# Kernel optimization log

Hardware: AMD Instinct MI355X
Metric: run time of the kernel (lower is better)

Reference implementation:

```python
import jax, jax.numpy as jnp
import numpy as np

B, T, I, H, N_LAYERS = 32, 1024, 512, 512, 4


def _custom_lstm(x, w, u, b):
    # x: [B,T,I]; w: [4,I,H] (gate order i,f,c,o); u: [4,H,H]; b: [4,H]
    # Preactivations for all timesteps/gates at once: [T,4,B,H]
    pre = jnp.einsum('bti,gih->tgbh', x, w) + b[None, :, None, :]
    h0 = jnp.zeros((x.shape[0], b.shape[-1]), x.dtype)
    c0 = jnp.zeros_like(h0)

    def step(carry, p):
        h, c = carry
        rec = jnp.einsum('bh,ghk->gbk', h, u)
        g = jax.nn.sigmoid(p + rec)          # all 4 gates use sigmoid (incl. g_t, as in source)
        i_t, f_t, g_t, o_t = g[0], g[1], g[2], g[3]
        c = f_t + c + i_t * g_t              # faithful: additive, not f*c
        h = o_t + jnp.tanh(c)                # faithful: additive, not o*tanh(c)
        return (h, c), h

    (h, c), hs = jax.lax.scan(step, (h0, c0), pre)
    return h, c, jnp.transpose(hs, (1, 0, 2))  # [B,T,H]


def _vlstm(x, h_prev, wx, wh, u, b):
    # x: [B,T,I]; h_prev: [B,T,H]; wx: [4,I,H]; wh: [4,H,H]; u: [4,H,H]; b: [4,H]
    # Source bug preserved: ALL gates use u[0] (u_i) and b[0] (b_i).
    pre = (jnp.einsum('bti,gih->tgbh', x, wx)
           + jnp.einsum('bth,ghk->tgbk', h_prev, wh)
           + b[0][None, None, None, :])
    u_i = u[0]
    h0 = jnp.zeros((x.shape[0], b.shape[-1]), x.dtype)
    c0 = jnp.zeros_like(h0)

    def step(carry, p):
        h, c = carry
        rec = h @ u_i                        # shared recurrent term for all gates
        g = jax.nn.sigmoid(p + rec[None])
        i_t, f_t, g_t, o_t = g[0], g[1], g[2], g[3]
        c = f_t + c + i_t * g_t
        h = o_t + jnp.tanh(c)
        return (h, c), h

    (h, c), hs = jax.lax.scan(step, (h0, c0), pre)
    return h, c, jnp.transpose(hs, (1, 0, 2))


def setup_inputs() -> dict:
    key = jax.random.key(0)
    ks = jax.random.split(key, 6)
    stdv = 1.0 / np.sqrt(H)
    u_ = lambda k, shp: jax.random.uniform(k, shp, jnp.float32, -stdv, stdv)
    L = N_LAYERS - 1
    return {
        'x': jax.random.normal(ks[0], (B, T, I), jnp.float32),
        'w1': u_(ks[1], (4, I, H)),
        'u1': u_(ks[2], (4, H, H)),
        'b1': u_(ks[3], (4, H)),
        'wx': u_(ks[4], (L, 4, I, H)),
        'wh': u_(ks[5], (L, 4, H, H)),
        'uv': u_(jax.random.fold_in(key, 10), (L, 4, H, H)),
        'bv': u_(jax.random.fold_in(key, 11), (L, 4, H)),
    }


def reference(x, w1, u1, b1, wx, wh, uv, bv):
    h_t, c_t, h_vec = _custom_lstm(x, w1, u1, b1)
    for l in range(wx.shape[0]):  # verbose path: each VLSTM sees raw x + prev layer h_vec
        h_t, c_t, h_vec = _vlstm(x, h_vec, wx[l], wh[l], uv[l], bv[l])
    return h_t, c_t, h_vec
```

## Files before the change

### kernel.cpp

```cpp
#include <hip/hip_runtime.h>

typedef unsigned short u16;
typedef unsigned int u32;
typedef unsigned long long u64;
typedef __attribute__((ext_vector_type(4))) float f32x4;
typedef __attribute__((ext_vector_type(8))) short short8;
typedef __attribute__((ext_vector_type(4))) short short4v;

__device__ __forceinline__ float bf2f(u16 v){ u32 b = ((u32)v)<<16; float f; __builtin_memcpy(&f,&b,4); return f; }
__device__ __forceinline__ u16 f2bf(float f){ u32 b; __builtin_memcpy(&b,&f,4); b = b + 0x7fffu + ((b>>16)&1u); return (u16)(b>>16); }
__device__ __forceinline__ float sigm(float x){ return 1.f/(1.f+__expf(-x)); }
__device__ __forceinline__ float tanh_a(float x){ return 1.f - 2.f/(__expf(2.f*x)+1.f); }
__device__ __forceinline__ int imin(int a, int b){ return a<b?a:b; }

typedef const __attribute__((address_space(1))) u32* gas1;
typedef __attribute__((address_space(3))) u32* las3;
__device__ __forceinline__ void gld16(const u16* g, u16* l){
  __builtin_amdgcn_global_load_lds((gas1)g, (las3)l, 16, 0, 0);
}

__device__ __forceinline__ void pub64(u32* p, u64 v){
  __hip_atomic_store((u64*)p, v, __ATOMIC_RELAXED, __HIP_MEMORY_SCOPE_AGENT);
}
__device__ __forceinline__ void pub32(u32* p, u32 v){
  __hip_atomic_store(p, v, __ATOMIC_RELAXED, __HIP_MEMORY_SCOPE_AGENT);
}
__device__ __forceinline__ u64 pol64(const u32* p){
  return __hip_atomic_load((const u64*)p, __ATOMIC_RELAXED, __HIP_MEMORY_SCOPE_AGENT);
}
__device__ __forceinline__ u32 pol32(const u32* p){
  return __hip_atomic_load(p, __ATOMIC_RELAXED, __HIP_MEMORY_SCOPE_AGENT);
}

__global__ void cast_x_kernel(const float* __restrict__ in, u16* __restrict__ out){
  int i = blockIdx.x*256 + threadIdx.x;
  for (; i < 4194304; i += 2048*256){
    f32x4 v = ((const f32x4*)in)[i];
    short4v o;
    o[0]=(short)f2bf(v[0]); o[1]=(short)f2bf(v[1]); o[2]=(short)f2bf(v[2]); o[3]=(short)f2bf(v[3]);
    ((short4v*)out)[i] = o;
  }
}

__global__ void pack_w_kernel(const float* __restrict__ w1, const float* __restrict__ wx, const float* __restrict__ wh,
                              u16* __restrict__ w1p, u16* __restrict__ wxwhp){
  int e = blockIdx.x*256 + threadIdx.x;
  for (; e < 7340032; e += 2048*256){
    if (e < 1048576){
      int h = e & 511, k = (e>>9)&511, g = e>>18;
      w1p[(size_t)(g*512+h)*512 + k] = f2bf(w1[(size_t)g*262144 + (size_t)k*512 + h]);
    } else {
      int r = e - 1048576;
      int lv = r >> 21;
      int q = r & 2097151;
      int n = q >> 10, k = q & 1023;
      int g = n >> 9, h = n & 511;
      float v;
      if (k < 512) v = wx[(size_t)lv*1048576 + (size_t)g*262144 + (size_t)k*512 + h];
      else         v = wh[(size_t)lv*1048576 + (size_t)g*262144 + (size_t)(k-512)*512 + h];
      wxwhp[(size_t)lv*2097152 + (size_t)n*1024 + k] = f2bf(v);
    }
  }
}

__global__ void cast_u_kernel(const float* __restrict__ u1, const float* __restrict__ uv,
                              u16* __restrict__ u1p, u16* __restrict__ uv0p){
  int e = blockIdx.x*256 + threadIdx.x;
  for (; e < 1835008; e += 1024*256){
    if (e < 1048576) u1p[e] = f2bf(u1[e]);
    else { int r = e - 1048576; uv0p[r] = f2bf(uv[(size_t)(r>>18)*1048576 + (r & 262143)]); }
  }
}

__global__ __launch_bounds__(256) void gemm_pre_kernel(
    const u16* __restrict__ A1, const u16* __restrict__ B1,
    const u16* __restrict__ A2, const u16* __restrict__ B2,
    const float* __restrict__ bias, int bmask,
    u16* __restrict__ Out, int nPass)
{
  __shared__ u16 As[128*64];
  __shared__ u16 Bs[128*64];
  const int tid = threadIdx.x;
  const int w = tid>>6, lane = tid&63;
  const int l15 = lane&15, l4 = lane>>4;
  const int m0 = blockIdx.x*128, n0 = blockIdx.y*128;
  const int wm = w>>1, wn = w&1;
  f32x4 acc[4][4];
#pragma unroll
  for (int a=0;a<4;a++)
#pragma unroll
    for (int bq=0;bq<4;bq++) acc[a][bq] = (f32x4){0.f,0.f,0.f,0.f};

  for (int p=0;p<nPass;p++){
    const u16* Ap = p ? A2 : A1;
    const u16* Bp = p ? B2 : B1;
    for (int kt=0;kt<8;kt++){
      const int k0 = kt*64;
      __syncthreads();
#pragma unroll
      for (int i=0;i<4;i++){
        int chunk = w*4 + i;
        int fb = chunk*1024 + lane*16;
        int row = fb>>7;
        int slot = (fb>>4)&7;
        const u16* srcA = Ap + (size_t)(m0+row)*512 + k0 + ((slot ^ (row&7))<<3);
        gld16(srcA, (u16*)As + chunk*512);
        const u16* srcB = Bp + (size_t)(n0+row)*512 + k0 + ((slot ^ (row&7))<<3);
        gld16(srcB, (u16*)Bs + chunk*512);
      }
      __syncthreads();
#pragma unroll
      for (int kk=0;kk<2;kk++){
        short8 af[4], bfq[4];
#pragma unroll
        for (int mi=0;mi<4;mi++){
          int row = wm*64 + mi*16 + l15;
          int s16 = l4 + kk*4;
          af[mi] = *(const short8*)&As[row*64 + ((s16 ^ (row&7))<<3)];
        }
#pragma unroll
        for (int ni=0;ni<4;ni++){
          int row = wn*64 + ni*16 + l15;
          int s16 = l4 + kk*4;
          bfq[ni] = *(const short8*)&Bs[row*64 + ((s16 ^ (row&7))<<3)];
        }
#pragma unroll
        for (int mi=0;mi<4;mi++)
#pragma unroll
          for (int ni=0;ni<4;ni++)
            acc[mi][ni] = __builtin_amdgcn_mfma_f32_16x16x32_bf16(af[mi], bfq[ni], acc[mi][ni], 0,0,0);
      }
    }
  }
#pragma unroll
  for (int ni=0;ni<4;ni++){
    int col = n0 + wn*64 + ni*16 + l15;
    float bb = bias[col & bmask];
#pragma unroll
    for (int mi=0;mi<4;mi++){
#pragma unroll
      for (int i=0;i<4;i++){
        int row = m0 + wm*64 + mi*16 + l4*4 + i;
        Out[(size_t)row*2048 + col] = f2bf(acc[mi][ni][i] + bb);
      }
    }
  }
}

__global__ __launch_bounds__(512,2) void mega_kernel(
    const u16* __restrict__ pre1, const u16* __restrict__ u1p,
    const u16* __restrict__ uv0p, const u16* __restrict__ xb,
    const u16* __restrict__ wxwhp, const float* __restrict__ bv,
    u32* hring, u32* pring, u32* prog, float* __restrict__ out)
{
  __shared__ char smem[33024];
  const int bid = blockIdx.x;
  const int tid = threadIdx.x;
  const int lane = tid&63, w = tid>>6;
  const int l15 = lane&15, l4 = lane>>4;

  if (bid < 16){
    u16* hs = (u16*)smem;
    float* recb = (float*)(smem+16384);
    const int gk = bid & 7, gb = bid >> 3;
    const int b0 = gb*16, kb = gk*64;
    const int g = w>>1, ch = w&1;
    short8 bfr[2][16];
#pragma unroll
    for (int n=0;n<2;n++){
      const u16* up = u1p + (size_t)g*262144 + (kb + ch*32 + n*16 + l15);
#pragma unroll
      for (int s=0;s<16;s++){
        int kbase = s*32 + l4*8;
#pragma unroll
        for (int j=0;j<8;j++) bfr[n][s][j] = (short)up[(size_t)(kbase+j)*512];
      }
    }
    { short8 z = {0,0,0,0,0,0,0,0};
      for (int i=tid;i<1024;i+=512) ((short8*)hs)[i]=z; }
    const int b = tid>>5, q = tid&31;
    const int hc2 = q*2;
    float cA=0.f, cB=0.f;
    __syncthreads();

    for (int t=0;t<1024;++t){
      if ((t&15)==0 && t>=32){
        int thr = t-32;
        for(;;){
          int m0=(int)pol32(&prog[0]); m0=imin(m0,(int)pol32(&prog[1]));
          m0=imin(m0,(int)pol32(&prog[2])); m0=imin(m0,(int)pol32(&prog[3]));
          if (m0>=thr) break;
          __builtin_amdgcn_s_sleep(8);
        }
      }
      const u16* prow = pre1 + ((size_t)((b0+b)*1024+t))*2048 + kb + hc2;
      u32 pw0 = *(const u32*)(prow);
      u32 pw1 = *(const u32*)(prow+512);
      u32 pw2 = *(const u32*)(prow+1024);
      u32 pw3 = *(const u32*)(prow+1536);
      f32x4 acc0 = {0.f,0.f,0.f,0.f}, acc1 = {0.f,0.f,0.f,0.f};
      {
        int rb = l15*512, sw = (l15&7)<<3;
#pragma unroll
        for (int s=0;s<16;s++){
          short8 a = *(const short8*)&hs[rb + ((s*32 + l4*8) ^ sw)];
          acc0 = __builtin_amdgcn_mfma_f32_16x16x32_bf16(a, bfr[0][s], acc0, 0,0,0);
          acc1 = __builtin_amdgcn_mfma_f32_16x16x32_bf16(a, bfr[1][s], acc1, 0,0,0);
        }
      }
      {
        int base = g*64 + ch*32 + l15;
#pragma unroll
        for (int i=0;i<4;i++){
          recb[(l4*4+i)*256 + base]      = acc0[i];
          recb[(l4*4+i)*256 + base + 16] = acc1[i];
        }
      }
      __syncthreads();
      float ri0 = recb[b*256 + hc2],       ri1 = recb[b*256 + hc2+1];
      float rf0 = recb[b*256 + 64 + hc2],  rf1 = recb[b*256 + 64 + hc2+1];
      float rg0 = recb[b*256 + 128 + hc2], rg1 = recb[b*256 + 128 + hc2+1];
      float ro0 = recb[b*256 + 192 + hc2], ro1 = recb[b*256 + 192 + hc2+1];
      float gi0 = sigm(bf2f((u16)(pw0&0xffffu)) + ri0), gi1 = sigm(bf2f((u16)(pw0>>16)) + ri1);
      float gf0 = sigm(bf2f((u16)(pw1&0xffffu)) + rf0), gf1 = sigm(bf2f((u16)(pw1>>16)) + rf1);
      float gg0 = sigm(bf2f((u16)(pw2&0xffffu)) + rg0), gg1 = sigm(bf2f((u16)(pw2>>16)) + rg1);
      float go0 = sigm(bf2f((u16)(pw3&0xffffu)) + ro0), go1 = sigm(bf2f((u16)(pw3>>16)) + ro1);
      cA = gf0 + cA + gi0*gg0; float h0v = go0 + tanh_a(cA);
      cB = gf1 + cB + gi1*gg1; float h1v = go1 + tanh_a(cB);
      u16 hb0 = f2bf(h0v), hb1 = f2bf(h1v);
      const u32 tag = (u32)(t+1);
      u32* slot = hring + (size_t)(t&63)*16384;
      u64 msg = (((u64)((tag<<16)|(u32)hb1))<<32) | (u64)((tag<<16)|(u32)hb0);
      pub64(&slot[(size_t)(b0+b)*512 + kb + hc2], msg);
      u32 hpair = (u32)hb0 | ((u32)hb1<<16);
      *(u32*)&hs[b*512 + ((kb+hc2) ^ ((b&7)<<3))] = hpair;
      {
        const u32* srcg = slot + (size_t)(b0+b)*512;
        u64 nv[7];
        for(;;){
#pragma unroll
          for (int j=0;j<7;j++){
            int fc = q*14 + 2*j;
            int ac = fc + (fc>=kb ? 64 : 0);
            nv[j] = pol64(&srcg[ac]);
          }
          u32 ok = 1;
#pragma unroll
          for (int j=0;j<7;j++){
            if ((u32)(((u32)nv[j])>>16) != tag) ok=0;
            if ((u32)(nv[j]>>48) != tag) ok=0;
          }
          if (ok) break;
          __builtin_amdgcn_s_sleep(1);
        }
#pragma unroll
        for (int j=0;j<7;j++){
          int fc = q*14 + 2*j;
          int ac = fc + (fc>=kb ? 64 : 0);
          u32 pair = ((u32)nv[j]&0xffffu) | ((u32)((nv[j]>>32)&0xffffu)<<16);
          *(u32*)&hs[b*512 + (ac ^ ((b&7)<<3))] = pair;
        }
      }
      __syncthreads();
    }
  } else if (bid < 28){
    u16* hs = (u16*)smem;
    float* recb = (float*)(smem+16384);
    const int l = 1 + ((bid-16)>>2);
    const int lv = l-1;
    const int sub = (bid-16)&3;
    const int ch = sub&1, gb = sub>>1;
    const int b0 = gb*16, cbase = ch*256;
    short8 bfr[2][16];
#pragma unroll
    for (int n=0;n<2;n++){
      const u16* up = uv0p + (size_t)lv*262144 + (cbase + w*32 + n*16 + l15);
#pragma unroll
      for (int s=0;s<16;s++){
        int kbase = s*32 + l4*8;
#pragma unroll
        for (int j=0;j<8;j++) bfr[n][s][j] = (short)up[(size_t)(kbase+j)*512];
      }
    }
    { short8 z = {0,0,0,0,0,0,0,0};
      for (int i=tid;i<1024;i+=512) ((short8*)hs)[i]=z; }
    const int b = tid>>5, q = tid&31;
    const int oc = cbase + q*8;
    float cv[8];
#pragma unroll
    for (int j=0;j<8;j++) cv[j]=0.f;
    u32* hr = hring + (size_t)l*1048576;
    u32* pr = pring + (size_t)lv*4194304;
    const int is_last = (l==3);
    __syncthreads();

    for (int t=0;t<1024;++t){
      const u32 tag = (u32)(t+1);
      if (l<3 && (t&15)==0 && t>=32){
        int thr=t-32;
        const int pbase = l*4;
        for(;;){
          int m0=(int)pol32(&prog[pbase]); m0=imin(m0,(int)pol32(&prog[pbase+1]));
          m0=imin(m0,(int)pol32(&prog[pbase+2])); m0=imin(m0,(int)pol32(&prog[pbase+3]));
          if (m0>=thr) break;
          __builtin_amdgcn_s_sleep(8);
        }
      }
      const u32* ps = pr + (size_t)(t&63)*65536 + (size_t)(b0+b)*2048;
      u64 pv[16];
#pragma unroll
      for (int gq=0;gq<4;gq++)
#pragma unroll
        for (int j=0;j<4;j++)
          pv[gq*4+j] = pol64(&ps[gq*512 + oc + 2*j]);
      f32x4 acc0={0.f,0.f,0.f,0.f}, acc1={0.f,0.f,0.f,0.f};
      {
        int rb=l15*512, sw=(l15&7)<<3;
#pragma unroll
        for (int s=0;s<16;s++){
          short8 a = *(const short8*)&hs[rb + ((s*32+l4*8)^sw)];
          acc0 = __builtin_amdgcn_mfma_f32_16x16x32_bf16(a, bfr[0][s], acc0, 0,0,0);
          acc1 = __builtin_amdgcn_mfma_f32_16x16x32_bf16(a, bfr[1][s], acc1, 0,0,0);
        }
      }
      {
        int base = w*32 + l15;
#pragma unroll
        for (int i=0;i<4;i++){
          recb[(l4*4+i)*256 + base]    = acc0[i];
          recb[(l4*4+i)*256 + base+16] = acc1[i];
        }
      }
      for(;;){
        u32 ok=1;
#pragma unroll
        for (int i=0;i<16;i++){
          if ((u32)(((u32)pv[i])>>16) != tag) ok=0;
          if ((u32)(pv[i]>>48) != tag) ok=0;
        }
        if (ok) break;
        __builtin_amdgcn_s_sleep(2);
#pragma unroll
        for (int gq=0;gq<4;gq++)
#pragma unroll
          for (int j=0;j<4;j++)
            pv[gq*4+j] = pol64(&ps[gq*512 + oc + 2*j]);
      }
      __syncthreads();
      short8 hvv; float hf[8]; u32 msgw[8];
#pragma unroll
      for (int j=0;j<8;j++){
        float r = recb[b*256 + q*8 + j];
        int wi = j>>1;
        u32 w0 = (j&1) ? (u32)(pv[wi]>>32)    : (u32)pv[wi];
        u32 w1v= (j&1) ? (u32)(pv[4+wi]>>32)  : (u32)pv[4+wi];
        u32 w2 = (j&1) ? (u32)(pv[8+wi]>>32)  : (u32)pv[8+wi];
        u32 w3 = (j&1) ? (u32)(pv[12+wi]>>32) : (u32)pv[12+wi];
        float gi = sigm(bf2f((u16)(w0&0xffffu)) + r);
        float gf = sigm(bf2f((u16)(w1v&0xffffu)) + r);
        float gg = sigm(bf2f((u16)(w2&0xffffu)) + r);
        float go = sigm(bf2f((u16)(w3&0xffffu)) + r);
        cv[j] = gf + cv[j] + gi*gg;
        float h = go + tanh_a(cv[j]);
        u16 hb = f2bf(h);
        hvv[j]=(short)hb; hf[j]=h; msgw[j] = (tag<<16)|(u32)hb;
      }
      u32* hslot = hr + (size_t)(t&63)*16384 + (size_t)(b0+b)*512;
#pragma unroll
      for (int j=0;j<4;j++){
        u64 m = (((u64)msgw[2*j+1])<<32) | (u64)msgw[2*j];
        pub64(&hslot[oc + 2*j], m);
      }
      *(short8*)&hs[b*512 + (oc ^ ((b&7)<<3))] = hvv;
      if (is_last){
        f32x4 h4a={hf[0],hf[1],hf[2],hf[3]}, h4b={hf[4],hf[5],hf[6],hf[7]};
        *(f32x4*)&out[32768 + ((size_t)((b0+b)*1024+t))*512 + oc]   = h4a;
        *(f32x4*)&out[32768 + ((size_t)((b0+b)*1024+t))*512 + oc+4] = h4b;
        if (t==1023){
          *(f32x4*)&out[(size_t)(b0+b)*512 + oc]   = h4a;
          *(f32x4*)&out[(size_t)(b0+b)*512 + oc+4] = h4b;
          f32x4 c4a={cv[0],cv[1],cv[2],cv[3]}, c4b={cv[4],cv[5],cv[6],cv[7]};
          *(f32x4*)&out[16384 + (size_t)(b0+b)*512 + oc]   = c4a;
          *(f32x4*)&out[16384 + (size_t)(b0+b)*512 + oc+4] = c4b;
        }
      }
      {
        const u32* src = hslot + (ch^1)*256 + q*8;
        u64 nv[4];
        for(;;){
#pragma unroll
          for (int j=0;j<4;j++) nv[j] = pol64(&src[2*j]);
          u32 ok=1;
#pragma unroll
          for (int j=0;j<4;j++){
            if ((u32)(((u32)nv[j])>>16)!=tag) ok=0;
            if ((u32)(nv[j]>>48)!=tag) ok=0;
          }
          if (ok) break;
          __builtin_amdgcn_s_sleep(1);
        }
        short8 hh;
#pragma unroll
        for (int j=0;j<4;j++){
          hh[2*j]   = (short)(u16)(nv[j] & 0xffffu);
          hh[2*j+1] = (short)(u16)((nv[j]>>32) & 0xffffu);
        }
        int pc = (ch^1)*256 + q*8;
        *(short8*)&hs[b*512 + (pc ^ ((b&7)<<3))] = hh;
      }
      __syncthreads();
      if (tid==0) pub32(&prog[(l-1)*4 + sub], (u32)(t+1));
    }
  } else {
    u16* hstage = (u16*)smem;
    const int idx = bid - 28;
    const int lv = idx >> 5;
    const int r  = idx & 31;
    const int gb = r & 1, cg = r >> 1;
    const int b0 = gb*16;
    const int c  = cg*128 + w*16 + l15;
    const u16* Bw = wxwhp + (size_t)lv*2097152 + (size_t)c*1024;
    short8 bfr[32];
#pragma unroll
    for (int s=0;s<32;s++) bfr[s] = *(const short8*)&Bw[s*32 + l4*8];
    const float bias = bv[lv*2048 + (c & 511)];
    const int prow_ = tid >> 5;
    const int px = tid & 31;
    const u32* hrb = hring + (size_t)lv*1048576;
    u32* prb = pring + (size_t)lv*4194304;

    for (int t=0;t<1024;++t){
      const u32 tag = (u32)(t+1);
      const u32* hsrc = hrb + (size_t)(t&63)*16384 + (size_t)(b0+prow_)*512;
      u64 nv[8];
#pragma unroll
      for (int j=0;j<8;j++) nv[j] = pol64(&hsrc[px*2 + 64*j]);
      f32x4 acc = {0.f,0.f,0.f,0.f};
      const u16* xrow = xb + ((size_t)(b0+l15)*1024 + t)*512;
#pragma unroll
      for (int s=0;s<16;s++){
        short8 a = *(const short8*)&xrow[s*32 + l4*8];
        acc = __builtin_amdgcn_mfma_f32_16x16x32_bf16(a, bfr[s], acc, 0,0,0);
      }
      for(;;){
        u32 ok=1;
#pragma unroll
        for (int j=0;j<8;j++){
          if ((u32)(((u32)nv[j])>>16)!=tag) ok=0;
          if ((u32)(nv[j]>>48)!=tag) ok=0;
        }
        if (ok) break;
        __builtin_amdgcn_s_sleep(2);
#pragma unroll
        for (int j=0;j<8;j++) nv[j] = pol64(&hsrc[px*2 + 64*j]);
      }
#pragma unroll
      for (int j=0;j<8;j++){
        u32 pair = ((u32)nv[j]&0xffffu) | ((u32)((nv[j]>>32)&0xffffu)<<16);
        *(u32*)&hstage[prow_*520 + px*2 + 64*j] = pair;
      }
      __syncthreads();
#pragma unroll
      for (int s=0;s<16;s++){
        short8 a = *(const short8*)&hstage[l15*520 + s*32 + l4*8];
        acc = __builtin_amdgcn_mfma_f32_16x16x32_bf16(a, bfr[16+s], acc, 0,0,0);
      }
      u32* dst = prb + (size_t)(t&63)*65536 + c;
#pragma unroll
      for (int i=0;i<4;i++){
        u32 v = ((u32)f2bf(acc[i]+bias)) | (tag<<16);
        pub32(&dst[(size_t)(b0 + l4*4 + i)*2048], v);
      }
      __syncthreads();
    }
  }
}

extern "C" void kernel_launch(void* const* d_in, const int* in_sizes, int n_in,
                              void* d_out, int out_size, void* d_ws, size_t ws_size,
                              hipStream_t stream)
{
  const float* x  = (const float*)d_in[0];
  const float* w1 = (const float*)d_in[1];
  const float* u1 = (const float*)d_in[2];
  const float* b1 = (const float*)d_in[3];
  const float* wx = (const float*)d_in[4];
  const float* wh = (const float*)d_in[5];
  const float* uv = (const float*)d_in[6];
  const float* bv = (const float*)d_in[7];
  float* out = (float*)d_out;

  char* p = (char*)d_ws;
  u16* pre1  = (u16*)p; p += (size_t)134217728;
  u16* xb    = (u16*)p; p += 33554432;
  u16* w1p   = (u16*)p; p += 2097152;
  u16* wxwhp = (u16*)p; p += 12582912;
  u16* u1p   = (u16*)p; p += 2097152;
  u16* uv0p  = (u16*)p; p += 1572864;
  u32* hring = (u32*)p; p += 16777216;
  u32* pring = (u32*)p; p += 50331648;
  u32* prog  = (u32*)p; p += 256;
  if ((size_t)(p - (char*)d_ws) > ws_size) return;

  hipMemsetAsync(hring, 0, 16777216, stream);
  hipMemsetAsync(pring, 0, 50331648, stream);
  hipMemsetAsync(prog, 0, 256, stream);
  cast_x_kernel<<<2048,256,0,stream>>>(x, xb);
  pack_w_kernel<<<2048,256,0,stream>>>(w1, wx, wh, w1p, wxwhp);
  cast_u_kernel<<<1024,256,0,stream>>>(u1, uv, u1p, uv0p);

  gemm_pre_kernel<<<dim3(256,16),256,0,stream>>>(xb, w1p, (const u16*)nullptr, (const u16*)nullptr, b1, 2047, pre1, 1);
  mega_kernel<<<124,512,0,stream>>>(pre1, u1p, uv0p, xb, wxwhp, bv, hring, pring, prog, out);
}
```

Baseline: 8.042 ms.

## Store x and preactivations time-major and add per-block progress flags for polling

The bf16 copy of x is written in [T,B,I] order, so the preactivation GEMM output becomes time-major. Per-step reads of pre1 and x rows in the recurrent mega kernel now touch contiguous rows for a given timestep. Blocks also publish per-step progress counters in an enlarged prog array. Consumers wait on those counters before re-polling the tagged h/preact ring slots, which is meant to cut polling traffic on the ring. The extra flag stores and polls add cross-block memory traffic and ordering assumptions.

```diff
diff --git a/kernel.cpp b/kernel.cpp
--- a/kernel.cpp
+++ b/kernel.cpp
@@ -36,9 +36,11 @@
   int i = blockIdx.x*256 + threadIdx.x;
   for (; i < 4194304; i += 2048*256){
     f32x4 v = ((const f32x4*)in)[i];
+    int e = i*4;
+    int b = e >> 19, t = (e >> 9) & 1023, k = e & 511;
     short4v o;
     o[0]=(short)f2bf(v[0]); o[1]=(short)f2bf(v[1]); o[2]=(short)f2bf(v[2]); o[3]=(short)f2bf(v[3]);
-    ((short4v*)out)[i] = o;
+    *(short4v*)&out[(size_t)(t*32+b)*512 + k] = o;
   }
 }
 
@@ -74,9 +76,8 @@
 
 __global__ __launch_bounds__(256) void gemm_pre_kernel(
     const u16* __restrict__ A1, const u16* __restrict__ B1,
-    const u16* __restrict__ A2, const u16* __restrict__ B2,
     const float* __restrict__ bias, int bmask,
-    u16* __restrict__ Out, int nPass)
+    u16* __restrict__ Out)
 {
   __shared__ u16 As[128*64];
   __shared__ u16 Bs[128*64];
@@ -91,45 +92,41 @@
 #pragma unroll
     for (int bq=0;bq<4;bq++) acc[a][bq] = (f32x4){0.f,0.f,0.f,0.f};
 
-  for (int p=0;p<nPass;p++){
-    const u16* Ap = p ? A2 : A1;
-    const u16* Bp = p ? B2 : B1;
-    for (int kt=0;kt<8;kt++){
-      const int k0 = kt*64;
-      __syncthreads();
-#pragma unroll
-      for (int i=0;i<4;i++){
-        int chunk = w*4 + i;
-        int fb = chunk*1024 + lane*16;
-        int row = fb>>7;
-        int slot = (fb>>4)&7;
-        const u16* srcA = Ap + (size_t)(m0+row)*512 + k0 + ((slot ^ (row&7))<<3);
-        gld16(srcA, (u16*)As + chunk*512);
-        const u16* srcB = Bp + (size_t)(n0+row)*512 + k0 + ((slot ^ (row&7))<<3);
-        gld16(srcB, (u16*)Bs + chunk*512);
-      }
-      __syncthreads();
-#pragma unroll
-      for (int kk=0;kk<2;kk++){
-        short8 af[4], bfq[4];
-#pragma unroll
-        for (int mi=0;mi<4;mi++){
-          int row = wm*64 + mi*16 + l15;
-          int s16 = l4 + kk*4;
-          af[mi] = *(const short8*)&As[row*64 + ((s16 ^ (row&7))<<3)];
-        }
-#pragma unroll
-        for (int ni=0;ni<4;ni++){
-          int row = wn*64 + ni*16 + l15;
-          int s16 = l4 + kk*4;
-          bfq[ni] = *(const short8*)&Bs[row*64 + ((s16 ^ (row&7))<<3)];
-        }
-#pragma unroll
-        for (int mi=0;mi<4;mi++)
-#pragma unroll
-          for (int ni=0;ni<4;ni++)
-            acc[mi][ni] = __builtin_amdgcn_mfma_f32_16x16x32_bf16(af[mi], bfq[ni], acc[mi][ni], 0,0,0);
-      }
+  for (int kt=0;kt<8;kt++){
+    const int k0 = kt*64;
+    __syncthreads();
+#pragma unroll
+    for (int i=0;i<4;i++){
+      int chunk = w*4 + i;
+      int fb = chunk*1024 + lane*16;
+      int row = fb>>7;
+      int slot = (fb>>4)&7;
+      const u16* srcA = A1 + (size_t)(m0+row)*512 + k0 + ((slot ^ (row&7))<<3);
+      gld16(srcA, (u16*)As + chunk*512);
+      const u16* srcB = B1 + (size_t)(n0+row)*512 + k0 + ((slot ^ (row&7))<<3);
+      gld16(srcB, (u16*)Bs + chunk*512);
+    }
+    __syncthreads();
+#pragma unroll
+    for (int kk=0;kk<2;kk++){
+      short8 af[4], bfq[4];
+#pragma unroll
+      for (int mi=0;mi<4;mi++){
+        int row = wm*64 + mi*16 + l15;
+        int s16 = l4 + kk*4;
+        af[mi] = *(const short8*)&As[row*64 + ((s16 ^ (row&7))<<3)];
+      }
+#pragma unroll
+      for (int ni=0;ni<4;ni++){
+        int row = wn*64 + ni*16 + l15;
+        int s16 = l4 + kk*4;
+        bfq[ni] = *(const short8*)&Bs[row*64 + ((s16 ^ (row&7))<<3)];
+      }
+#pragma unroll
+      for (int mi=0;mi<4;mi++)
+#pragma unroll
+        for (int ni=0;ni<4;ni++)
+          acc[mi][ni] = __builtin_amdgcn_mfma_f32_16x16x32_bf16(af[mi], bfq[ni], acc[mi][ni], 0,0,0);
     }
   }
 #pragma unroll
@@ -193,7 +190,7 @@
           __builtin_amdgcn_s_sleep(8);
         }
       }
-      const u16* prow = pre1 + ((size_t)((b0+b)*1024+t))*2048 + kb + hc2;
+      const u16* prow = pre1 + ((size_t)(t*32 + b0 + b))*2048 + kb + hc2;
       u32 pw0 = *(const u32*)(prow);
       u32 pw1 = *(const u32*)(prow+512);
       u32 pw2 = *(const u32*)(prow+1024);
@@ -262,6 +259,7 @@
         }
       }
       __syncthreads();
+      if (tid==0) pub32(&prog[32+bid], (u32)(t+1));
     }
   } else if (bid < 28){
     u16* hs = (u16*)smem;
@@ -339,7 +337,17 @@
           if ((u32)(pv[i]>>48) != tag) ok=0;
         }
         if (ok) break;
-        __builtin_amdgcn_s_sleep(2);
+        for(;;){
+          int mn = 0x7fffffff;
+#pragma unroll
+          for (int g=0; g<4; g++){
+            int cg0 = g*4 + ch*2;
+            mn = imin(mn, (int)pol32(&prog[64 + lv*32 + (cg0*2+gb)]));
+            mn = imin(mn, (int)pol32(&prog[64 + lv*32 + ((cg0+1)*2+gb)]));
+          }
+          if (mn >= (int)tag) break;
+          __builtin_amdgcn_s_sleep(4);
+        }
 #pragma unroll
         for (int gq=0;gq<4;gq++)
 #pragma unroll
@@ -436,7 +444,7 @@
 #pragma unroll
       for (int j=0;j<8;j++) nv[j] = pol64(&hsrc[px*2 + 64*j]);
       f32x4 acc = {0.f,0.f,0.f,0.f};
-      const u16* xrow = xb + ((size_t)(b0+l15)*1024 + t)*512;
+      const u16* xrow = xb + (size_t)(t*32 + b0 + l15)*512;
 #pragma unroll
       for (int s=0;s<16;s++){
         short8 a = *(const short8*)&xrow[s*32 + l4*8];
@@ -450,7 +458,22 @@
           if ((u32)(nv[j]>>48)!=tag) ok=0;
         }
         if (ok) break;
-        __builtin_amdgcn_s_sleep(2);
+        if (lv==0){
+          for(;;){
+            int mn = 0x7fffffff;
+#pragma unroll
+            for (int j=0;j<8;j++) mn = imin(mn, (int)pol32(&prog[32 + gb*8 + j]));
+            if (mn >= (int)tag) break;
+            __builtin_amdgcn_s_sleep(4);
+          }
+        } else {
+          for(;;){
+            int a2 = (int)pol32(&prog[(lv-1)*4 + gb*2]);
+            int c2 = (int)pol32(&prog[(lv-1)*4 + gb*2 + 1]);
+            if (imin(a2,c2) >= (int)tag) break;
+            __builtin_amdgcn_s_sleep(4);
+          }
+        }
 #pragma unroll
         for (int j=0;j<8;j++) nv[j] = pol64(&hsrc[px*2 + 64*j]);
       }
@@ -472,6 +495,7 @@
         pub32(&dst[(size_t)(b0 + l4*4 + i)*2048], v);
       }
       __syncthreads();
+      if (tid==0) pub32(&prog[64 + lv*32 + r], (u32)(t+1));
     }
   }
 }
@@ -499,16 +523,16 @@
   u16* uv0p  = (u16*)p; p += 1572864;
   u32* hring = (u32*)p; p += 16777216;
   u32* pring = (u32*)p; p += 50331648;
-  u32* prog  = (u32*)p; p += 256;
+  u32* prog  = (u32*)p; p += 1024;
   if ((size_t)(p - (char*)d_ws) > ws_size) return;
 
   hipMemsetAsync(hring, 0, 16777216, stream);
   hipMemsetAsync(pring, 0, 50331648, stream);
-  hipMemsetAsync(prog, 0, 256, stream);
+  hipMemsetAsync(prog, 0, 1024, stream);
   cast_x_kernel<<<2048,256,0,stream>>>(x, xb);
   pack_w_kernel<<<2048,256,0,stream>>>(w1, wx, wh, w1p, wxwhp);
   cast_u_kernel<<<1024,256,0,stream>>>(u1, uv, u1p, uv0p);
 
-  gemm_pre_kernel<<<dim3(256,16),256,0,stream>>>(xb, w1p, (const u16*)nullptr, (const u16*)nullptr, b1, 2047, pre1, 1);
+  gemm_pre_kernel<<<dim3(256,16),256,0,stream>>>(xb, w1p, b1, 2047, pre1);
   mega_kernel<<<124,512,0,stream>>>(pre1, u1p, uv0p, xb, wxwhp, bv, hring, pring, prog, out);
 }
```

After: 7.624 ms. 1.05x faster.
